# Performance work log

Measured on AMD Instinct MI355X. Metric: run time of the kernel, lower is better.

Reference implementation:

```python
import jax, jax.numpy as jnp
import numpy as np

N_NODES = 50000
N_EDGES = 200000
N_TASK = 10000
VOCAB = 1000
D = 64
H = 4
C = 64  # per-head dim (out_channels)


def setup_inputs() -> dict:
    key = jax.random.key(0)
    ks = jax.random.split(key, 16)
    s = 0.05
    return {
        "x": jax.random.randint(ks[0], (N_NODES,), 0, VOCAB),
        "edge_index": jax.random.randint(ks[1], (2, N_EDGES), 0, N_NODES),
        "task_idx": jax.random.randint(ks[2], (N_TASK,), 0, N_NODES),
        "emb": jax.random.normal(ks[3], (VOCAB, D), jnp.float32) * s,
        "Wq": jax.random.normal(ks[4], (D, H * C), jnp.float32) * s,
        "bq": jax.random.normal(ks[5], (H * C,), jnp.float32) * s,
        "Wk": jax.random.normal(ks[6], (D, H * C), jnp.float32) * s,
        "bk": jax.random.normal(ks[7], (H * C,), jnp.float32) * s,
        "Wv": jax.random.normal(ks[8], (D, H * C), jnp.float32) * s,
        "bv": jax.random.normal(ks[9], (H * C,), jnp.float32) * s,
        "Wskip": jax.random.normal(ks[10], (D, D), jnp.float32) * s,
        "bskip": jax.random.normal(ks[11], (D,), jnp.float32) * s,
        "Wbeta": jax.random.normal(ks[12], (3 * D, 1), jnp.float32) * s,
        "W1": jax.random.normal(ks[13], (D, 32), jnp.float32) * s,
        "b1": jax.random.normal(ks[14], (32,), jnp.float32) * s,
        "W2": jax.random.normal(ks[15], (32, 1), jnp.float32) * s,
        "b2": jnp.zeros((1,), jnp.float32),
    }


def _transformer_conv(h, src, dst, Wq, bq, Wk, bk, Wv, bv, Wskip, bskip, Wbeta):
    N = h.shape[0]
    q = (h @ Wq + bq).reshape(N, H, C)
    k = (h @ Wk + bk).reshape(N, H, C)
    v = (h @ Wv + bv).reshape(N, H, C)
    # per-edge gather: message from src j to dst i
    qe = q[dst]            # [E,H,C]
    ke = k[src]
    ve = v[src]
    scale = 1.0 / jnp.sqrt(jnp.float32(C))
    alpha = jnp.sum(qe * ke, axis=-1) * scale  # [E,H]
    # segment softmax over destination node
    m = jax.ops.segment_max(alpha, dst, num_segments=N)      # [N,H]
    e = jnp.exp(alpha - m[dst])
    denom = jax.ops.segment_sum(e, dst, num_segments=N)      # [N,H]
    a = e / denom[dst]                                       # [E,H]
    msg = ve * a[..., None]                                  # [E,H,C]
    out = jax.ops.segment_sum(msg, dst, num_segments=N)      # [N,H,C]
    out = out.mean(axis=1)                                   # concat=False -> mean over heads
    x_r = h @ Wskip + bskip
    beta = jax.nn.sigmoid(jnp.concatenate([out, x_r, out - x_r], axis=-1) @ Wbeta)  # [N,1]
    return beta * x_r + (1.0 - beta) * out


def reference(x, edge_index, task_idx, emb, Wq, bq, Wk, bk, Wv, bv, Wskip, bskip, Wbeta, W1, b1, W2, b2):
    h = emb[x]  # [N,D]
    src, dst = edge_index[0], edge_index[1]
    h = _transformer_conv(h, src, dst, Wq, bq, Wk, bk, Wv, bv, Wskip, bskip, Wbeta)
    hs = h[task_idx]  # [T,D]
    risk = jax.nn.sigmoid(jax.nn.relu(hs @ W1 + b1) @ W2 + b2)  # dropout = identity (eval)
    return risk.squeeze(-1)
```

## Files before the change

### kernel.cpp

```cpp
#include <hip/hip_runtime.h>
#include <hip/hip_bf16.h>
#include <math.h>

#define N_NODES 50000
#define N_EDGES 200000
#define N_TASK  10000
#define VOCAB   1000
#define HC      256
#define CAP     32

__global__ __launch_bounds__(256) void k_tables(
    const float* __restrict__ emb,
    const float* __restrict__ Wq, const float* __restrict__ bq,
    const float* __restrict__ Wk, const float* __restrict__ bk,
    const float* __restrict__ Wv, const float* __restrict__ bv,
    const float* __restrict__ Wskip, const float* __restrict__ bskip,
    const int* __restrict__ task,
    float* __restrict__ qtab, float* __restrict__ ktab,
    float* __restrict__ vtab, float* __restrict__ xrtab,
    int* __restrict__ cursor) {
  int b = blockIdx.x;
  int tid = threadIdx.x;
  if (b >= 125) {
    int i = (b - 125) * 256 + tid;
    if (i < N_TASK) cursor[task[i]] = 0;
    return;
  }
  __shared__ float hs[8 * 64];
  int v0 = b * 8;
  hs[tid]       = emb[v0 * 64 + tid];
  hs[tid + 256] = emb[v0 * 64 + 256 + tid];
  __syncthreads();

  float aq[8], ak[8], av[8];
#pragma unroll
  for (int r = 0; r < 8; r++) { aq[r] = 0.f; ak[r] = 0.f; av[r] = 0.f; }
  for (int d = 0; d < 64; d++) {
    float wq = Wq[d * 256 + tid];
    float wk = Wk[d * 256 + tid];
    float wv = Wv[d * 256 + tid];
#pragma unroll
    for (int r = 0; r < 8; r++) {
      float h = hs[r * 64 + d];
      aq[r] += h * wq; ak[r] += h * wk; av[r] += h * wv;
    }
  }
#pragma unroll
  for (int r = 0; r < 8; r++) {
    qtab[(v0 + r) * 256 + tid] = aq[r] + bq[tid];
    ktab[(v0 + r) * 256 + tid] = ak[r] + bk[tid];
    vtab[(v0 + r) * 256 + tid] = av[r] + bv[tid];
  }
  if (tid < 64) {
    float as[8];
#pragma unroll
    for (int r = 0; r < 8; r++) as[r] = 0.f;
    for (int d = 0; d < 64; d++) {
      float w = Wskip[d * 64 + tid];
#pragma unroll
      for (int r = 0; r < 8; r++) as[r] += hs[r * 64 + d] * w;
    }
#pragma unroll
    for (int r = 0; r < 8; r++) xrtab[(v0 + r) * 64 + tid] = as[r] + bskip[tid];
  }
}

__global__ __launch_bounds__(256) void k_fill(
    const int* __restrict__ ei, const int* __restrict__ x,
    int* __restrict__ cursor, int* __restrict__ ecsr) {
  int e = blockIdx.x * 256 + threadIdx.x;
  if (e >= N_EDGES) return;
  int dst = ei[N_EDGES + e];
  int slot = atomicAdd(&cursor[dst], 1);
  if ((unsigned)slot < CAP) ecsr[dst * CAP + slot] = x[ei[e]];
}

__global__ __launch_bounds__(256) void k_task(
    const int* __restrict__ task, const int* __restrict__ x,
    const int* __restrict__ cursor, const int* __restrict__ ecsr,
    const float* __restrict__ qtab, const float* __restrict__ ktab,
    const float* __restrict__ vtab, const float* __restrict__ xrtab,
    const float* __restrict__ Wbeta, const float* __restrict__ W1,
    const float* __restrict__ b1, const float* __restrict__ W2,
    const float* __restrict__ b2, float* __restrict__ out) {
  int t = (blockIdx.x * blockDim.x + threadIdx.x) >> 6;
  if (t >= N_TASK) return;
  const int lane = threadIdx.x & 63;
  const int j = lane & 15;
  const int r = lane >> 4;

  int node = task[t];
  int xd = x[node];
  int dc = cursor[node];
  if (dc > CAP) dc = CAP;
  int sv = (lane < dc) ? ecsr[node * CAP + lane] : 0;
  float4 q4 = ((const float4*)(qtab + (size_t)xd * HC))[lane];
  float4 xr = ((const float4*)(xrtab + (size_t)xd * 64))[j];

  float4 w0 = ((const float4*)(Wbeta))[j];
  float4 w1 = ((const float4*)(Wbeta + 64))[j];
  float4 w2 = ((const float4*)(Wbeta + 128))[j];
  float4 wbA = make_float4(w0.x + w2.x, w0.y + w2.y, w0.z + w2.z, w0.w + w2.w);
  float4 wbB = make_float4(w1.x - w2.x, w1.y - w2.y, w1.z - w2.z, w1.w - w2.w);
  float w1v[4][8];
#pragma unroll
  for (int di = 0; di < 4; di++)
#pragma unroll
    for (int ki = 0; ki < 8; ki++)
      w1v[di][ki] = W1[(4 * j + di) * 32 + 8 * r + ki];
  float b1v[8], w2v[8];
#pragma unroll
  for (int ki = 0; ki < 8; ki++) { b1v[ki] = b1[8 * r + ki]; w2v[ki] = W2[8 * r + ki]; }
  const float b2s = b2[0];

  float denom = 0.f;
  float4 num = make_float4(0.f, 0.f, 0.f, 0.f);
  for (int i = 0; i < dc; i++) {
    int xs = __shfl(sv, i);
    float4 k4 = ((const float4*)(ktab + (size_t)xs * HC))[lane];
    float4 v4 = ((const float4*)(vtab + (size_t)xs * HC))[lane];
    float p = q4.x * k4.x + q4.y * k4.y + q4.z * k4.z + q4.w * k4.w;
    p += __shfl_xor(p, 1);
    p += __shfl_xor(p, 2);
    p += __shfl_xor(p, 4);
    p += __shfl_xor(p, 8);
    float ev = __expf(p * 0.125f);
    num.x += ev * v4.x; num.y += ev * v4.y;
    num.z += ev * v4.z; num.w += ev * v4.w;
    denom += ev;
  }
  float inv = (dc > 0) ? (1.f / denom) : 0.f;
  float4 om = make_float4(num.x * inv, num.y * inv, num.z * inv, num.w * inv);
  om.x += __shfl_xor(om.x, 16); om.y += __shfl_xor(om.y, 16);
  om.z += __shfl_xor(om.z, 16); om.w += __shfl_xor(om.w, 16);
  om.x += __shfl_xor(om.x, 32); om.y += __shfl_xor(om.y, 32);
  om.z += __shfl_xor(om.z, 32); om.w += __shfl_xor(om.w, 32);
  om.x *= 0.25f; om.y *= 0.25f; om.z *= 0.25f; om.w *= 0.25f;
  float p = om.x * wbA.x + om.y * wbA.y + om.z * wbA.z + om.w * wbA.w
          + xr.x * wbB.x + xr.y * wbB.y + xr.z * wbB.z + xr.w * wbB.w;
  p += __shfl_xor(p, 1);
  p += __shfl_xor(p, 2);
  p += __shfl_xor(p, 4);
  p += __shfl_xor(p, 8);
  float beta = 1.f / (1.f + __expf(-p));
  float4 hv = make_float4(beta * xr.x + (1.f - beta) * om.x,
                          beta * xr.y + (1.f - beta) * om.y,
                          beta * xr.z + (1.f - beta) * om.z,
                          beta * xr.w + (1.f - beta) * om.w);
  float part[8];
#pragma unroll
  for (int ki = 0; ki < 8; ki++)
    part[ki] = hv.x * w1v[0][ki] + hv.y * w1v[1][ki]
             + hv.z * w1v[2][ki] + hv.w * w1v[3][ki];
#pragma unroll
  for (int o = 1; o < 16; o <<= 1) {
#pragma unroll
    for (int ki = 0; ki < 8; ki++) part[ki] += __shfl_xor(part[ki], o);
  }
  float z = 0.f;
#pragma unroll
  for (int ki = 0; ki < 8; ki++) z += fmaxf(part[ki] + b1v[ki], 0.f) * w2v[ki];
  z += __shfl_xor(z, 16);
  z += __shfl_xor(z, 32);
  if (lane == 0) out[t] = 1.f / (1.f + __expf(-(z + b2s)));
}

extern "C" void kernel_launch(void* const* d_in, const int* in_sizes, int n_in,
                              void* d_out, int out_size, void* d_ws, size_t ws_size,
                              hipStream_t stream) {
  const int*   x     = (const int*)d_in[0];
  const int*   ei    = (const int*)d_in[1];
  const int*   task  = (const int*)d_in[2];
  const float* emb   = (const float*)d_in[3];
  const float* Wq    = (const float*)d_in[4];
  const float* bq    = (const float*)d_in[5];
  const float* Wk    = (const float*)d_in[6];
  const float* bk    = (const float*)d_in[7];
  const float* Wv    = (const float*)d_in[8];
  const float* bv    = (const float*)d_in[9];
  const float* Wskip = (const float*)d_in[10];
  const float* bskip = (const float*)d_in[11];
  const float* Wbeta = (const float*)d_in[12];
  const float* W1    = (const float*)d_in[13];
  const float* b1    = (const float*)d_in[14];
  const float* W2    = (const float*)d_in[15];
  const float* b2    = (const float*)d_in[16];
  float* out = (float*)d_out;

  char* ws = (char*)d_ws;
  size_t off = 0;
  auto alloc = [&](size_t bytes) {
    size_t o = off;
    off += (bytes + 255) & ~(size_t)255;
    return o;
  };
  int*   cursor = (int*)(ws + alloc(sizeof(int) * N_NODES));
  int*   ecsr   = (int*)(ws + alloc(sizeof(int) * (size_t)N_NODES * CAP));
  float* qtab   = (float*)(ws + alloc(sizeof(float) * VOCAB * HC));
  float* ktab   = (float*)(ws + alloc(sizeof(float) * VOCAB * HC));
  float* vtab   = (float*)(ws + alloc(sizeof(float) * VOCAB * HC));
  float* xrtab  = (float*)(ws + alloc(sizeof(float) * VOCAB * 64));
  (void)ws_size; (void)n_in; (void)in_sizes; (void)out_size;

  k_tables<<<165, 256, 0, stream>>>(emb, Wq, bq, Wk, bk, Wv, bv, Wskip, bskip,
                                    task, qtab, ktab, vtab, xrtab, cursor);

  k_fill<<<(N_EDGES + 255) / 256, 256, 0, stream>>>(ei, x, cursor, ecsr);

  k_task<<<(N_TASK * 64 + 255) / 256, 256, 0, stream>>>(
      task, x, cursor, ecsr, qtab, ktab, vtab, xrtab,
      Wbeta, W1, b1, W2, b2, out);
}
```

Measured before the change: 135.6 us.

## Fuse edge fill into table kernel and split cursor reset into its own kernel

The edge bucketing (fill) work now runs as extra blocks of the projection-table kernel, so table construction and edge scattering overlap in one launch. The cursor reset for task nodes moves into a small separate kernel that runs first. Each fill thread now handles 4 edges using vectorized int4 loads. A cursor read now guards each atomic, so the atomic is skipped when the cursor is negative. That check adds a load per edge and only saves atomics if the workspace happens to hold negative values.

```diff
diff --git a/kernel.cpp b/kernel.cpp
--- a/kernel.cpp
+++ b/kernel.cpp
@@ -9,23 +9,46 @@
 #define HC      256
 #define CAP     32
 
-__global__ __launch_bounds__(256) void k_tables(
+__global__ __launch_bounds__(256) void k_scatter(
+    const int* __restrict__ task, int* __restrict__ cursor) {
+  int i = blockIdx.x * 256 + threadIdx.x;
+  if (i < N_TASK) cursor[task[i]] = 0;
+}
+
+#define FILL_B0 125
+#define FILL_NB 196
+
+__global__ __launch_bounds__(256) void k_tables_fill(
     const float* __restrict__ emb,
     const float* __restrict__ Wq, const float* __restrict__ bq,
     const float* __restrict__ Wk, const float* __restrict__ bk,
     const float* __restrict__ Wv, const float* __restrict__ bv,
     const float* __restrict__ Wskip, const float* __restrict__ bskip,
-    const int* __restrict__ task,
+    const int* __restrict__ ei, const int* __restrict__ x,
     float* __restrict__ qtab, float* __restrict__ ktab,
     float* __restrict__ vtab, float* __restrict__ xrtab,
-    int* __restrict__ cursor) {
-  int b = blockIdx.x;
-  int tid = threadIdx.x;
-  if (b >= 125) {
-    int i = (b - 125) * 256 + tid;
-    if (i < N_TASK) cursor[task[i]] = 0;
+    int* __restrict__ cursor, int* __restrict__ ecsr) {
+  const int b = blockIdx.x;
+  const int tid = threadIdx.x;
+
+  if (b >= FILL_B0) {
+    int base = (b - FILL_B0) * 1024 + tid * 4;
+    if (base >= N_EDGES) return;
+    int4 d4 = *(const int4*)(ei + N_EDGES + base);
+    int4 s4 = *(const int4*)(ei + base);
+    int dsts[4] = {d4.x, d4.y, d4.z, d4.w};
+    int srcs[4] = {s4.x, s4.y, s4.z, s4.w};
+#pragma unroll
+    for (int u = 0; u < 4; u++) {
+      int dst = dsts[u];
+      if (cursor[dst] >= 0) {
+        int slot = atomicAdd(&cursor[dst], 1);
+        if (slot < CAP) ecsr[dst * CAP + slot] = x[srcs[u]];
+      }
+    }
     return;
   }
+
   __shared__ float hs[8 * 64];
   int v0 = b * 8;
   hs[tid]       = emb[v0 * 64 + tid];
@@ -63,16 +86,6 @@
 #pragma unroll
     for (int r = 0; r < 8; r++) xrtab[(v0 + r) * 64 + tid] = as[r] + bskip[tid];
   }
-}
-
-__global__ __launch_bounds__(256) void k_fill(
-    const int* __restrict__ ei, const int* __restrict__ x,
-    int* __restrict__ cursor, int* __restrict__ ecsr) {
-  int e = blockIdx.x * 256 + threadIdx.x;
-  if (e >= N_EDGES) return;
-  int dst = ei[N_EDGES + e];
-  int slot = atomicAdd(&cursor[dst], 1);
-  if ((unsigned)slot < CAP) ecsr[dst * CAP + slot] = x[ei[e]];
 }
 
 __global__ __launch_bounds__(256) void k_task(
@@ -202,10 +215,11 @@
   float* xrtab  = (float*)(ws + alloc(sizeof(float) * VOCAB * 64));
   (void)ws_size; (void)n_in; (void)in_sizes; (void)out_size;
 
-  k_tables<<<165, 256, 0, stream>>>(emb, Wq, bq, Wk, bk, Wv, bv, Wskip, bskip,
-                                    task, qtab, ktab, vtab, xrtab, cursor);
-
-  k_fill<<<(N_EDGES + 255) / 256, 256, 0, stream>>>(ei, x, cursor, ecsr);
+  k_scatter<<<(N_TASK + 255) / 256, 256, 0, stream>>>(task, cursor);
+
+  k_tables_fill<<<FILL_B0 + FILL_NB, 256, 0, stream>>>(
+      emb, Wq, bq, Wk, bk, Wv, bv, Wskip, bskip, ei, x,
+      qtab, ktab, vtab, xrtab, cursor, ecsr);
 
   k_task<<<(N_TASK * 64 + 255) / 256, 256, 0, stream>>>(
       task, x, cursor, ecsr, qtab, ktab, vtab, xrtab,
```

Result: no change. 133.3 us (-1.7%).
